# Performance work log

Measured on AMD Instinct MI355X. Metric: run time of the kernel, lower is better.

The kernel has to match this reference:

```python
import jax, jax.numpy as jnp
import numpy as np

N_NODES = 50000
N_EDGES = 800000
IN_C, HID_C, OUT_C = 128, 256, 128


def _gcn_conv(x, src, dst, W, b, num_nodes):
    # PyG GCNConv: self-loops + symmetric normalization + linear + scatter-add
    deg = jax.ops.segment_sum(jnp.ones_like(src, x.dtype), dst, num_segments=num_nodes)
    dinv = jnp.where(deg > 0, jax.lax.rsqrt(deg), 0.0)
    norm = dinv[src] * dinv[dst]                      # [E']
    h = x @ W.T                                       # [N, C_out] transform first (C_out usually < C_in path cost)
    msg = h[src] * norm[:, None]                      # [E', C_out] gather + scale
    out = jax.ops.segment_sum(msg, dst, num_segments=num_nodes)  # scatter-add
    return out + b


def setup_inputs() -> dict:
    key = jax.random.key(0)
    k1, k2, k3, k4 = jax.random.split(key, 4)
    x = jax.random.normal(k1, (N_NODES, IN_C), dtype=jnp.float32)
    edge_index = jax.random.randint(k2, (2, N_EDGES), 0, N_NODES, dtype=jnp.int64)
    W1 = jax.random.normal(k3, (HID_C, IN_C), dtype=jnp.float32) * (1.0 / np.sqrt(IN_C))
    b1 = jnp.zeros((HID_C,), dtype=jnp.float32)
    W2 = jax.random.normal(k4, (OUT_C, HID_C), dtype=jnp.float32) * (1.0 / np.sqrt(HID_C))
    b2 = jnp.zeros((OUT_C,), dtype=jnp.float32)
    return {"x": x, "edge_index": edge_index, "W1": W1, "b1": b1,
            "W2": W2, "b2": b2, "num_nodes": N_NODES}


def reference(x, edge_index, W1, b1, W2, b2, num_nodes):
    # add self-loops once (shared by both layers)
    loop = jnp.arange(num_nodes, dtype=edge_index.dtype)
    src = jnp.concatenate([edge_index[0], loop])
    dst = jnp.concatenate([edge_index[1], loop])
    h = _gcn_conv(x, src, dst, W1, b1, num_nodes)
    h = jax.nn.relu(h)
    out = _gcn_conv(h, src, dst, W2, b2, num_nodes)
    return out
```

## Files before the change

kernel.cpp:

```cpp
#include <hip/hip_runtime.h>

#define N_NODES 50000
#define N_EDGES 800000
#define IN_C 128
#define HID_C 256
#define OUT_C 128
#define NBLK 196
#define NPART 8
#define NREP 8
#define REP_W (N_EDGES / NREP)
#define EB 3125
#define XCONV_BLKS 6250
#define WCONV_BLKS 64

typedef __attribute__((ext_vector_type(8))) short short8v;
typedef __attribute__((ext_vector_type(4))) float f32x4;

static __device__ __forceinline__ unsigned short f2bf(float f) {
  unsigned int u = __float_as_uint(f);
  unsigned int r = (u + 0x7fffu + ((u >> 16) & 1u)) >> 16;
  return (unsigned short)r;
}
static __device__ __forceinline__ float bf2f(unsigned short h) {
  return __uint_as_float(((unsigned int)h) << 16);
}
static __device__ __forceinline__ unsigned int packBF2(float a, float b) {
  return (unsigned int)f2bf(a) | ((unsigned int)f2bf(b) << 16);
}

__global__ __launch_bounds__(256) void deg_zero_k(int* __restrict__ deg8) {
  const int i = blockIdx.x * 256 + threadIdx.x;
  if (i < NREP * N_NODES) deg8[i] = 0;
}

__global__ __launch_bounds__(256) void convert_conv_k(
    const int* __restrict__ ei, uint2* __restrict__ edata, int* __restrict__ deg8,
    const float* __restrict__ x, unsigned int* __restrict__ xbf,
    const float* __restrict__ W1, unsigned int* __restrict__ w1bf,
    const float* __restrict__ W2, unsigned int* __restrict__ w2bf) {
  const int b = blockIdx.x;
  if (b < EB) {
    __shared__ int s_is64;
    if (threadIdx.x == 0) {
      int nz = 0;
#pragma unroll
      for (int k = 0; k < 64; ++k) nz |= ei[2 * k + 1];
      s_is64 = (nz == 0) ? 1 : 0;
    }
    __syncthreads();
    const int is64 = s_is64;
    const int e = b * 256 + threadIdx.x;
    if (e < N_EDGES) {
      int s, d;
      if (is64) {
        const uint2 sv = ((const uint2*)ei)[e];
        const uint2 dv = ((const uint2*)ei)[N_EDGES + e];
        s = (int)sv.x;
        d = (int)dv.x;
      } else {
        s = ei[e];
        d = ei[N_EDGES + e];
      }
      const int rep = e / REP_W;
      const int lrank = atomicAdd(&deg8[rep * N_NODES + d], 1);
      const uint2 t = {(unsigned int)d | ((unsigned int)lrank << 16) |
                           ((unsigned int)rep << 29),
                       (unsigned int)s};
      edata[e] = t;
    }
  } else if (b < EB + XCONV_BLKS) {
    const int i = (b - EB) * 256 + threadIdx.x;
    const float4 f = *(const float4*)(x + (long)i * 4);
    uint2 u = {packBF2(f.x, f.y), packBF2(f.z, f.w)};
    *(uint2*)(xbf + (long)i * 2) = u;
  } else if (b < EB + XCONV_BLKS + WCONV_BLKS) {
    const int i = (b - EB - XCONV_BLKS) * 256 + threadIdx.x;
    const float2 f = *(const float2*)(W1 + (long)i * 2);
    w1bf[i] = packBF2(f.x, f.y);
  } else {
    const int i = (b - EB - XCONV_BLKS - WCONV_BLKS) * 256 + threadIdx.x;
    const float2 f = *(const float2*)(W2 + (long)i * 2);
    w2bf[i] = packBF2(f.x, f.y);
  }
}

__global__ __launch_bounds__(256) void bsum_k(const int* __restrict__ deg8,
                                              int* __restrict__ bsum) {
  const int i = blockIdx.x * 256 + threadIdx.x;
  int v = 0;
  if (i < N_NODES) {
#pragma unroll
    for (int r = 0; r < NREP; ++r) v += deg8[r * N_NODES + i];
  }
#pragma unroll
  for (int off = 32; off > 0; off >>= 1) v += __shfl_down(v, off, 64);
  __shared__ int ws[4];
  if ((threadIdx.x & 63) == 0) ws[threadIdx.x >> 6] = v;
  __syncthreads();
  if (threadIdx.x == 0) bsum[blockIdx.x] = ws[0] + ws[1] + ws[2] + ws[3];
}

__global__ __launch_bounds__(256) void bscan_k(const int* __restrict__ bsum,
                                               int* __restrict__ boff) {
  __shared__ int s[256];
  const int t = threadIdx.x;
  const int v = (t < NBLK) ? bsum[t] : 0;
  s[t] = v;
  __syncthreads();
  for (int off = 1; off < 256; off <<= 1) {
    const int tmp = (t >= off) ? s[t - off] : 0;
    __syncthreads();
    s[t] += tmp;
    __syncthreads();
  }
  if (t < NBLK) boff[t] = s[t] - v;
}

__global__ __launch_bounds__(256) void bfinal_k(const int* __restrict__ deg8,
                                                const int* __restrict__ boff,
                                                int* __restrict__ rowstart,
                                                float* __restrict__ dinv,
                                                int* __restrict__ repoff) {
  __shared__ int s[256];
  const int t = threadIdx.x;
  const int i = blockIdx.x * 256 + t;
  int dr[NREP];
  int dtot = 0;
  if (i < N_NODES) {
#pragma unroll
    for (int r = 0; r < NREP; ++r) {
      dr[r] = deg8[r * N_NODES + i];
      dtot += dr[r];
    }
  }
  s[t] = dtot;
  __syncthreads();
  for (int off = 1; off < 256; off <<= 1) {
    const int tmp = (t >= off) ? s[t - off] : 0;
    __syncthreads();
    s[t] += tmp;
    __syncthreads();
  }
  const int run = boff[blockIdx.x] + s[t] - dtot;
  if (i < N_NODES) {
    rowstart[i] = run;
    dinv[i] = rsqrtf((float)dtot + 1.0f);
    int acc = run;
#pragma unroll
    for (int r = 0; r < NREP; ++r) {
      repoff[i * NREP + r] = acc;
      acc += dr[r];
    }
    if (i == N_NODES - 1) rowstart[N_NODES] = run + dtot;
  }
}

__global__ __launch_bounds__(256) void fill_csr_part_k(const uint2* __restrict__ edata,
                                                       const int* __restrict__ repoff,
                                                       int* __restrict__ csr_src) {
  const int p = blockIdx.x & 7;
  const int e = (blockIdx.x >> 3) * 256 + threadIdx.x;
  if (e < N_EDGES) {
    const uint2 t = edata[e];
    const int d = t.x & 0xffff;
    if (d / 6250 == p) {
      const int lrank = (t.x >> 16) & 0x1fff;
      const int rep = (int)(t.x >> 29);
      csr_src[repoff[d * NREP + rep] + lrank] = (int)t.y;
    }
  }
}

__global__ __launch_bounds__(256) void gemm_fused_k(
    const unsigned int* __restrict__ X,
    const unsigned int* __restrict__ W1BF,
    const float* __restrict__ b1,
    const unsigned int* __restrict__ W2BF,
    unsigned int* __restrict__ outBF) {
  constexpr int KP1 = 68;
  constexpr int HP = 132;
  __shared__ unsigned int xs[64 * KP1];
  __shared__ unsigned int h1s[64 * HP];

  const int tid = threadIdx.x;
  const int w = tid >> 6;
  const int l = tid & 63;
  const long nbase = (long)blockIdx.x * 64;
  const int kg = (l >> 4) * 8;
  const int lr = l & 15;
  const int mq0 = (l >> 4) * 4;

#pragma unroll
  for (int i = 0; i < 4; ++i) {
    const int idx = (tid + i * 256) * 4;
    const int row = idx >> 6, col = idx & 63;
    long gr = nbase + row;
    if (gr > N_NODES - 1) gr = N_NODES - 1;
    const uint4 v = *(const uint4*)(X + gr * 64 + col);
    *(uint4*)(xs + row * KP1 + col) = v;
  }
  __syncthreads();

  {
    const int m0w = w * 64;
    f32x4 acc[4][4];
#pragma unroll
    for (int nt = 0; nt < 4; ++nt)
#pragma unroll
      for (int mt = 0; mt < 4; ++mt) acc[nt][mt] = {0.0f, 0.0f, 0.0f, 0.0f};

#pragma unroll
    for (int ks = 0; ks < 4; ++ks) {
      const int ko = ks * 32 + kg;
      short8v wb[4];
#pragma unroll
      for (int mt = 0; mt < 4; ++mt)
        wb[mt] = *(const short8v*)(W1BF + (long)(m0w + mt * 16 + lr) * (IN_C / 2) +
                                   ko / 2);
#pragma unroll
      for (int nt = 0; nt < 4; ++nt) {
        const short8v xb = *(const short8v*)(xs + (nt * 16 + lr) * KP1 + ko / 2);
#pragma unroll
        for (int mt = 0; mt < 4; ++mt)
          acc[nt][mt] = __builtin_amdgcn_mfma_f32_16x16x32_bf16(wb[mt], xb,
                                                               acc[nt][mt], 0, 0, 0);
      }
    }

#pragma unroll
    for (int nt = 0; nt < 4; ++nt) {
      const int nl = nt * 16 + lr;
#pragma unroll
      for (int mt = 0; mt < 4; ++mt) {
        const int mq = m0w + mt * 16 + mq0;
        const float4 bv = *(const float4*)(b1 + mq);
        const float v0 = fmaxf(acc[nt][mt][0] + bv.x, 0.0f);
        const float v1 = fmaxf(acc[nt][mt][1] + bv.y, 0.0f);
        const float v2 = fmaxf(acc[nt][mt][2] + bv.z, 0.0f);
        const float v3 = fmaxf(acc[nt][mt][3] + bv.w, 0.0f);
        uint2 o = {packBF2(v0, v1), packBF2(v2, v3)};
        *(uint2*)(h1s + nl * HP + mq / 2) = o;
      }
    }
  }
  __syncthreads();

  {
    const int m0w = w * 32;
    f32x4 acc[4][2];
#pragma unroll
    for (int nt = 0; nt < 4; ++nt)
#pragma unroll
      for (int mt = 0; mt < 2; ++mt) acc[nt][mt] = {0.0f, 0.0f, 0.0f, 0.0f};

#pragma unroll
    for (int ks = 0; ks < 8; ++ks) {
      const int ko = ks * 32 + kg;
      short8v wb[2];
#pragma unroll
      for (int mt = 0; mt < 2; ++mt)
        wb[mt] = *(const short8v*)(W2BF + (long)(m0w + mt * 16 + lr) * (HID_C / 2) +
                                   ko / 2);
#pragma unroll
      for (int nt = 0; nt < 4; ++nt) {
        const short8v xb = *(const short8v*)(h1s + (nt * 16 + lr) * HP + ko / 2);
#pragma unroll
        for (int mt = 0; mt < 2; ++mt)
          acc[nt][mt] = __builtin_amdgcn_mfma_f32_16x16x32_bf16(wb[mt], xb,
                                                               acc[nt][mt], 0, 0, 0);
      }
    }

#pragma unroll
    for (int nt = 0; nt < 4; ++nt) {
      const long n = nbase + nt * 16 + lr;
      if (n < N_NODES) {
#pragma unroll
        for (int mt = 0; mt < 2; ++mt) {
          const int mq = m0w + mt * 16 + mq0;
          uint2 o = {packBF2(acc[nt][mt][0], acc[nt][mt][1]),
                     packBF2(acc[nt][mt][2], acc[nt][mt][3])};
          *(uint2*)(outBF + n * (OUT_C / 2) + mq / 2) = o;
        }
      }
    }
  }
}

template <int C, bool HAS_BIAS, bool OUT_BF>
__global__ __launch_bounds__(256) void gather_k(const int* __restrict__ rowstart,
                                                const int* __restrict__ csr_src,
                                                const float* __restrict__ dinv,
                                                const unsigned int* __restrict__ hbf,
                                                const float* __restrict__ bias,
                                                float* __restrict__ out,
                                                unsigned int* __restrict__ outBF) {
  const int v = (blockIdx.x * 256 + threadIdx.x) >> 6;
  if (v >= N_NODES) return;
  const int lane = threadIdx.x & 63;
  constexpr int CW = C / 2;
  const int rs = rowstart[v];
  const int re = rowstart[v + 1];
  const float dv = dinv[v];

  float a0 = 0.0f, a1 = 0.0f;

  int e = rs;
  for (; e + 7 < re; e += 8) {
    int s[8];
    float nn[8];
    unsigned int r[8];
#pragma unroll
    for (int j = 0; j < 8; ++j) s[j] = csr_src[e + j];
#pragma unroll
    for (int j = 0; j < 8; ++j) nn[j] = dv * dinv[s[j]];
#pragma unroll
    for (int j = 0; j < 8; ++j) r[j] = hbf[(long)s[j] * CW + lane];
#pragma unroll
    for (int j = 0; j < 8; ++j) {
      a0 += nn[j] * bf2f((unsigned short)r[j]);
      a1 += nn[j] * bf2f((unsigned short)(r[j] >> 16));
    }
  }
  for (; e + 3 < re; e += 4) {
    int s[4];
    float nn[4];
    unsigned int r[4];
#pragma unroll
    for (int j = 0; j < 4; ++j) s[j] = csr_src[e + j];
#pragma unroll
    for (int j = 0; j < 4; ++j) nn[j] = dv * dinv[s[j]];
#pragma unroll
    for (int j = 0; j < 4; ++j) r[j] = hbf[(long)s[j] * CW + lane];
#pragma unroll
    for (int j = 0; j < 4; ++j) {
      a0 += nn[j] * bf2f((unsigned short)r[j]);
      a1 += nn[j] * bf2f((unsigned short)(r[j] >> 16));
    }
  }
  for (; e < re; ++e) {
    const int s0 = csr_src[e];
    const float n0 = dv * dinv[s0];
    const unsigned int r0 = hbf[(long)s0 * CW + lane];
    a0 += n0 * bf2f((unsigned short)r0);
    a1 += n0 * bf2f((unsigned short)(r0 >> 16));
  }

  const float s2 = dv * dv;
  const unsigned int hv = hbf[(long)v * CW + lane];
  float o0 = s2 * bf2f((unsigned short)hv) + a0;
  float o1 = s2 * bf2f((unsigned short)(hv >> 16)) + a1;
  if (HAS_BIAS) {
    const float2 bv = *(const float2*)(bias + lane * 2);
    o0 += bv.x;
    o1 += bv.y;
  }
  if (OUT_BF) {
    outBF[(long)v * CW + lane] = packBF2(o0, o1);
  } else {
    const float2 o = {o0, o1};
    *(float2*)(out + (long)v * CW * 2 + lane * 2) = o;
  }
}

extern "C" void kernel_launch(void* const* d_in, const int* in_sizes, int n_in,
                              void* d_out, int out_size, void* d_ws, size_t ws_size,
                              hipStream_t stream) {
  (void)in_sizes; (void)n_in; (void)out_size; (void)ws_size;

  const float* x  = (const float*)d_in[0];
  const int*   ei = (const int*)d_in[1];
  const float* W1 = (const float*)d_in[2];
  const float* b1 = (const float*)d_in[3];
  const float* W2 = (const float*)d_in[4];
  const float* b2 = (const float*)d_in[5];
  float* out = (float*)d_out;

  char* ws = (char*)d_ws;
  uint2* edata    = (uint2*)(ws + 0);
  int*   csr_src  = (int*)(ws + 6400000);
  int*   deg8     = (int*)(ws + 9600000);
  int*   rowstart = (int*)(ws + 11200000);
  float* dinv     = (float*)(ws + 11400016);
  int*   bsum     = (int*)(ws + 11600016);
  int*   boff     = (int*)(ws + 11601040);
  int*   repoff   = (int*)(ws + 11700000);
  unsigned int* w1bf   = (unsigned int*)(ws + 13400000);
  unsigned int* w2bf   = (unsigned int*)(ws + 13500000);
  unsigned int* aggxbf = (unsigned int*)(ws + 14000000);
  unsigned int* h2bf   = (unsigned int*)(ws + 27000000);
  unsigned int* xbf    = (unsigned int*)(ws + 91200000);

  const int GB = (N_NODES + 3) / 4;

  deg_zero_k<<<(NREP * N_NODES + 255) / 256, 256, 0, stream>>>(deg8);
  convert_conv_k<<<EB + XCONV_BLKS + 2 * WCONV_BLKS, 256, 0, stream>>>(
      ei, edata, deg8, x, xbf, W1, w1bf, W2, w2bf);
  bsum_k<<<NBLK, 256, 0, stream>>>(deg8, bsum);
  bscan_k<<<1, 256, 0, stream>>>(bsum, boff);
  bfinal_k<<<NBLK, 256, 0, stream>>>(deg8, boff, rowstart, dinv, repoff);
  fill_csr_part_k<<<EB * NPART, 256, 0, stream>>>(edata, repoff, csr_src);

  gather_k<IN_C, false, true><<<GB, 256, 0, stream>>>(
      rowstart, csr_src, dinv, xbf, nullptr, nullptr, aggxbf);

  gemm_fused_k<<<(N_NODES + 63) / 64, 256, 0, stream>>>(aggxbf, w1bf, b1, w2bf,
                                                        h2bf);

  gather_k<OUT_C, true, false><<<GB, 256, 0, stream>>>(
      rowstart, csr_src, dinv, h2bf, b2, out, nullptr);
}
```

Measured before the change: 167.8 us.

## Build CSR via destination-partitioned buckets with LDS histograms instead of global atomics

```diff
diff --git a/kernel.cpp b/kernel.cpp
--- a/kernel.cpp
+++ b/kernel.cpp
@@ -7,8 +7,9 @@
 #define OUT_C 128
 #define NBLK 196
 #define NPART 8
-#define NREP 8
-#define REP_W (N_EDGES / NREP)
+#define PART_W 6250
+#define PCAP 110000
+#define KB 16
 #define EB 3125
 #define XCONV_BLKS 6250
 #define WCONV_BLKS 64
@@ -28,19 +29,24 @@
   return (unsigned int)f2bf(a) | ((unsigned int)f2bf(b) << 16);
 }
 
-__global__ __launch_bounds__(256) void deg_zero_k(int* __restrict__ deg8) {
-  const int i = blockIdx.x * 256 + threadIdx.x;
-  if (i < NREP * N_NODES) deg8[i] = 0;
-}
-
-__global__ __launch_bounds__(256) void convert_conv_k(
-    const int* __restrict__ ei, uint2* __restrict__ edata, int* __restrict__ deg8,
+__global__ void zero8_k(int* __restrict__ pcount) {
+  if (threadIdx.x < NPART) pcount[threadIdx.x] = 0;
+}
+
+__global__ __launch_bounds__(256) void partition_conv_k(
+    const int* __restrict__ ei, unsigned int* __restrict__ partbuf,
+    int* __restrict__ pcount,
     const float* __restrict__ x, unsigned int* __restrict__ xbf,
     const float* __restrict__ W1, unsigned int* __restrict__ w1bf,
     const float* __restrict__ W2, unsigned int* __restrict__ w2bf) {
   const int b = blockIdx.x;
   if (b < EB) {
     __shared__ int s_is64;
+    __shared__ int cnt[NPART], base[NPART], cur[NPART];
+    if (threadIdx.x < NPART) {
+      cnt[threadIdx.x] = 0;
+      cur[threadIdx.x] = 0;
+    }
     if (threadIdx.x == 0) {
       int nz = 0;
 #pragma unroll
@@ -50,8 +56,9 @@
     __syncthreads();
     const int is64 = s_is64;
     const int e = b * 256 + threadIdx.x;
-    if (e < N_EDGES) {
-      int s, d;
+    int s = 0, d = 0, p = 0;
+    const bool valid = (e < N_EDGES);
+    if (valid) {
       if (is64) {
         const uint2 sv = ((const uint2*)ei)[e];
         const uint2 dv = ((const uint2*)ei)[N_EDGES + e];
@@ -61,12 +68,20 @@
         s = ei[e];
         d = ei[N_EDGES + e];
       }
-      const int rep = e / REP_W;
-      const int lrank = atomicAdd(&deg8[rep * N_NODES + d], 1);
-      const uint2 t = {(unsigned int)d | ((unsigned int)lrank << 16) |
-                           ((unsigned int)rep << 29),
-                       (unsigned int)s};
-      edata[e] = t;
+      p = d / PART_W;
+      atomicAdd(&cnt[p], 1);
+    }
+    __syncthreads();
+    if (threadIdx.x < NPART)
+      base[threadIdx.x] = atomicAdd(&pcount[threadIdx.x], cnt[threadIdx.x]);
+    __syncthreads();
+    if (valid) {
+      const int o = atomicAdd(&cur[p], 1);
+      const int idx = base[p] + o;
+      if (idx < PCAP) {
+        partbuf[p * PCAP + idx] =
+            (unsigned int)(d - p * PART_W) | ((unsigned int)s << 13);
+      }
     }
   } else if (b < EB + XCONV_BLKS) {
     const int i = (b - EB) * 256 + threadIdx.x;
@@ -84,13 +99,36 @@
   }
 }
 
-__global__ __launch_bounds__(256) void bsum_k(const int* __restrict__ deg8,
+__global__ __launch_bounds__(1024) void hist_k(const unsigned int* __restrict__ partbuf,
+                                               const int* __restrict__ pcount,
+                                               int* __restrict__ H) {
+  const int p = blockIdx.x & 7;
+  const int blk = blockIdx.x >> 3;
+  __shared__ unsigned int hist[PART_W];
+  for (int i = threadIdx.x; i < PART_W; i += 1024) hist[i] = 0;
+  __syncthreads();
+  const int np = pcount[p] < PCAP ? pcount[p] : PCAP;
+  const int chunk = (np + KB - 1) / KB;
+  const int s0 = blk * chunk;
+  int s1 = s0 + chunk;
+  if (s1 > np) s1 = np;
+  const unsigned int* pb = partbuf + p * PCAP;
+  for (int i = s0 + threadIdx.x; i < s1; i += 1024)
+    atomicAdd(&hist[pb[i] & 0x1fffu], 1u);
+  __syncthreads();
+  int* Hrow = H + (p * KB + blk) * PART_W;
+  for (int i = threadIdx.x; i < PART_W; i += 1024) Hrow[i] = (int)hist[i];
+}
+
+__global__ __launch_bounds__(256) void bsum_k(const int* __restrict__ H,
                                               int* __restrict__ bsum) {
   const int i = blockIdx.x * 256 + threadIdx.x;
   int v = 0;
   if (i < N_NODES) {
-#pragma unroll
-    for (int r = 0; r < NREP; ++r) v += deg8[r * N_NODES + i];
+    const int p = i / PART_W, bin = i % PART_W;
+    const int* Hp = H + p * KB * PART_W + bin;
+#pragma unroll
+    for (int blk = 0; blk < KB; ++blk) v += Hp[blk * PART_W];
   }
 #pragma unroll
   for (int off = 32; off > 0; off >>= 1) v += __shfl_down(v, off, 64);
@@ -116,22 +154,21 @@
   if (t < NBLK) boff[t] = s[t] - v;
 }
 
-__global__ __launch_bounds__(256) void bfinal_k(const int* __restrict__ deg8,
+__global__ __launch_bounds__(256) void bfinal_k(int* __restrict__ H,
                                                 const int* __restrict__ boff,
                                                 int* __restrict__ rowstart,
-                                                float* __restrict__ dinv,
-                                                int* __restrict__ repoff) {
+                                                float* __restrict__ dinv) {
   __shared__ int s[256];
   const int t = threadIdx.x;
   const int i = blockIdx.x * 256 + t;
-  int dr[NREP];
   int dtot = 0;
+  int p = 0, bin = 0;
   if (i < N_NODES) {
-#pragma unroll
-    for (int r = 0; r < NREP; ++r) {
-      dr[r] = deg8[r * N_NODES + i];
-      dtot += dr[r];
-    }
+    p = i / PART_W;
+    bin = i % PART_W;
+    int* Hp = H + p * KB * PART_W + bin;
+#pragma unroll
+    for (int blk = 0; blk < KB; ++blk) dtot += Hp[blk * PART_W];
   }
   s[t] = dtot;
   __syncthreads();
@@ -146,28 +183,38 @@
     rowstart[i] = run;
     dinv[i] = rsqrtf((float)dtot + 1.0f);
     int acc = run;
-#pragma unroll
-    for (int r = 0; r < NREP; ++r) {
-      repoff[i * NREP + r] = acc;
-      acc += dr[r];
+    int* Hp = H + p * KB * PART_W + bin;
+#pragma unroll
+    for (int blk = 0; blk < KB; ++blk) {
+      const int c = Hp[blk * PART_W];
+      Hp[blk * PART_W] = acc;
+      acc += c;
     }
     if (i == N_NODES - 1) rowstart[N_NODES] = run + dtot;
   }
 }
 
-__global__ __launch_bounds__(256) void fill_csr_part_k(const uint2* __restrict__ edata,
-                                                       const int* __restrict__ repoff,
-                                                       int* __restrict__ csr_src) {
+__global__ __launch_bounds__(1024) void scatter_k(const unsigned int* __restrict__ partbuf,
+                                                  const int* __restrict__ pcount,
+                                                  const int* __restrict__ H,
+                                                  int* __restrict__ csr_src) {
   const int p = blockIdx.x & 7;
-  const int e = (blockIdx.x >> 3) * 256 + threadIdx.x;
-  if (e < N_EDGES) {
-    const uint2 t = edata[e];
-    const int d = t.x & 0xffff;
-    if (d / 6250 == p) {
-      const int lrank = (t.x >> 16) & 0x1fff;
-      const int rep = (int)(t.x >> 29);
-      csr_src[repoff[d * NREP + rep] + lrank] = (int)t.y;
-    }
+  const int blk = blockIdx.x >> 3;
+  __shared__ unsigned int hist[PART_W];
+  for (int i = threadIdx.x; i < PART_W; i += 1024) hist[i] = 0;
+  __syncthreads();
+  const int np = pcount[p] < PCAP ? pcount[p] : PCAP;
+  const int chunk = (np + KB - 1) / KB;
+  const int s0 = blk * chunk;
+  int s1 = s0 + chunk;
+  if (s1 > np) s1 = np;
+  const unsigned int* pb = partbuf + p * PCAP;
+  const int* Hrow = H + (p * KB + blk) * PART_W;
+  for (int i = s0 + threadIdx.x; i < s1; i += 1024) {
+    const unsigned int u = pb[i];
+    const int ld = (int)(u & 0x1fffu);
+    const int lr = (int)atomicAdd(&hist[ld], 1u);
+    csr_src[Hrow[ld] + lr] = (int)(u >> 13);
   }
 }
 
@@ -377,29 +424,30 @@
   float* out = (float*)d_out;
 
   char* ws = (char*)d_ws;
-  uint2* edata    = (uint2*)(ws + 0);
-  int*   csr_src  = (int*)(ws + 6400000);
-  int*   deg8     = (int*)(ws + 9600000);
-  int*   rowstart = (int*)(ws + 11200000);
-  float* dinv     = (float*)(ws + 11400016);
-  int*   bsum     = (int*)(ws + 11600016);
-  int*   boff     = (int*)(ws + 11601040);
-  int*   repoff   = (int*)(ws + 11700000);
-  unsigned int* w1bf   = (unsigned int*)(ws + 13400000);
-  unsigned int* w2bf   = (unsigned int*)(ws + 13500000);
-  unsigned int* aggxbf = (unsigned int*)(ws + 14000000);
-  unsigned int* h2bf   = (unsigned int*)(ws + 27000000);
+  unsigned int* partbuf = (unsigned int*)(ws + 0);
+  int*   csr_src  = (int*)(ws + 3600000);
+  int*   H        = (int*)(ws + 6800000);
+  int*   pcount   = (int*)(ws + 10000000);
+  int*   rowstart = (int*)(ws + 10000128);
+  float* dinv     = (float*)(ws + 10200640);
+  int*   bsum     = (int*)(ws + 10400640);
+  int*   boff     = (int*)(ws + 10401664);
+  unsigned int* w1bf   = (unsigned int*)(ws + 10500000);
+  unsigned int* w2bf   = (unsigned int*)(ws + 10600000);
+  unsigned int* aggxbf = (unsigned int*)(ws + 11000000);
+  unsigned int* h2bf   = (unsigned int*)(ws + 24000000);
   unsigned int* xbf    = (unsigned int*)(ws + 91200000);
 
   const int GB = (N_NODES + 3) / 4;
 
-  deg_zero_k<<<(NREP * N_NODES + 255) / 256, 256, 0, stream>>>(deg8);
-  convert_conv_k<<<EB + XCONV_BLKS + 2 * WCONV_BLKS, 256, 0, stream>>>(
-      ei, edata, deg8, x, xbf, W1, w1bf, W2, w2bf);
-  bsum_k<<<NBLK, 256, 0, stream>>>(deg8, bsum);
+  zero8_k<<<1, 64, 0, stream>>>(pcount);
+  partition_conv_k<<<EB + XCONV_BLKS + 2 * WCONV_BLKS, 256, 0, stream>>>(
+      ei, partbuf, pcount, x, xbf, W1, w1bf, W2, w2bf);
+  hist_k<<<NPART * KB, 1024, 0, stream>>>(partbuf, pcount, H);
+  bsum_k<<<NBLK, 256, 0, stream>>>(H, bsum);
   bscan_k<<<1, 256, 0, stream>>>(bsum, boff);
-  bfinal_k<<<NBLK, 256, 0, stream>>>(deg8, boff, rowstart, dinv, repoff);
-  fill_csr_part_k<<<EB * NPART, 256, 0, stream>>>(edata, repoff, csr_src);
+  bfinal_k<<<NBLK, 256, 0, stream>>>(H, boff, rowstart, dinv);
+  scatter_k<<<NPART * KB, 1024, 0, stream>>>(partbuf, pcount, H, csr_src);
 
   gather_k<IN_C, false, true><<<GB, 256, 0, stream>>>(
       rowstart, csr_src, dinv, xbf, nullptr, nullptr, aggxbf);
```

After: 167.9 us. No clear change (+0.1%).

## Build CSR with LDS-histogram partitioned counting instead of global atomics

Applied to the files above, without the earlier changes.

```diff
diff --git a/kernel.cpp b/kernel.cpp
--- a/kernel.cpp
+++ b/kernel.cpp
@@ -7,8 +7,9 @@
 #define OUT_C 128
 #define NBLK 196
 #define NPART 8
-#define NREP 8
-#define REP_W (N_EDGES / NREP)
+#define PART_W 6250
+#define KB2 32
+#define CHUNK (N_EDGES / KB2)
 #define EB 3125
 #define XCONV_BLKS 6250
 #define WCONV_BLKS 64
@@ -28,13 +29,8 @@
   return (unsigned int)f2bf(a) | ((unsigned int)f2bf(b) << 16);
 }
 
-__global__ __launch_bounds__(256) void deg_zero_k(int* __restrict__ deg8) {
-  const int i = blockIdx.x * 256 + threadIdx.x;
-  if (i < NREP * N_NODES) deg8[i] = 0;
-}
-
 __global__ __launch_bounds__(256) void convert_conv_k(
-    const int* __restrict__ ei, uint2* __restrict__ edata, int* __restrict__ deg8,
+    const int* __restrict__ ei, unsigned int* __restrict__ edata,
     const float* __restrict__ x, unsigned int* __restrict__ xbf,
     const float* __restrict__ W1, unsigned int* __restrict__ w1bf,
     const float* __restrict__ W2, unsigned int* __restrict__ w2bf) {
@@ -61,12 +57,7 @@
         s = ei[e];
         d = ei[N_EDGES + e];
       }
-      const int rep = e / REP_W;
-      const int lrank = atomicAdd(&deg8[rep * N_NODES + d], 1);
-      const uint2 t = {(unsigned int)d | ((unsigned int)lrank << 16) |
-                           ((unsigned int)rep << 29),
-                       (unsigned int)s};
-      edata[e] = t;
+      edata[e] = (unsigned int)d | ((unsigned int)s << 16);
     }
   } else if (b < EB + XCONV_BLKS) {
     const int i = (b - EB) * 256 + threadIdx.x;
@@ -84,13 +75,33 @@
   }
 }
 
-__global__ __launch_bounds__(256) void bsum_k(const int* __restrict__ deg8,
+__global__ __launch_bounds__(1024) void hist_k(const unsigned int* __restrict__ edata,
+                                               int* __restrict__ H) {
+  const int p = blockIdx.x & 7;
+  const int c = blockIdx.x >> 3;
+  __shared__ unsigned int hist[PART_W];
+  for (int i = threadIdx.x; i < PART_W; i += 1024) hist[i] = 0;
+  __syncthreads();
+  const int s0 = c * CHUNK;
+  for (int i = s0 + threadIdx.x; i < s0 + CHUNK; i += 1024) {
+    const unsigned int u = edata[i];
+    const int d = (int)(u & 0xffffu);
+    if (d / PART_W == p) atomicAdd(&hist[d - p * PART_W], 1u);
+  }
+  __syncthreads();
+  int* Hrow = H + (p * KB2 + c) * PART_W;
+  for (int i = threadIdx.x; i < PART_W; i += 1024) Hrow[i] = (int)hist[i];
+}
+
+__global__ __launch_bounds__(256) void bsum_k(const int* __restrict__ H,
                                               int* __restrict__ bsum) {
   const int i = blockIdx.x * 256 + threadIdx.x;
   int v = 0;
   if (i < N_NODES) {
-#pragma unroll
-    for (int r = 0; r < NREP; ++r) v += deg8[r * N_NODES + i];
+    const int p = i / PART_W, bin = i % PART_W;
+    const int* Hp = H + p * KB2 * PART_W + bin;
+#pragma unroll
+    for (int c = 0; c < KB2; ++c) v += Hp[c * PART_W];
   }
 #pragma unroll
   for (int off = 32; off > 0; off >>= 1) v += __shfl_down(v, off, 64);
@@ -116,22 +127,21 @@
   if (t < NBLK) boff[t] = s[t] - v;
 }
 
-__global__ __launch_bounds__(256) void bfinal_k(const int* __restrict__ deg8,
+__global__ __launch_bounds__(256) void bfinal_k(int* __restrict__ H,
                                                 const int* __restrict__ boff,
                                                 int* __restrict__ rowstart,
-                                                float* __restrict__ dinv,
-                                                int* __restrict__ repoff) {
+                                                float* __restrict__ dinv) {
   __shared__ int s[256];
   const int t = threadIdx.x;
   const int i = blockIdx.x * 256 + t;
-  int dr[NREP];
   int dtot = 0;
+  int p = 0, bin = 0;
   if (i < N_NODES) {
-#pragma unroll
-    for (int r = 0; r < NREP; ++r) {
-      dr[r] = deg8[r * N_NODES + i];
-      dtot += dr[r];
-    }
+    p = i / PART_W;
+    bin = i % PART_W;
+    int* Hp = H + p * KB2 * PART_W + bin;
+#pragma unroll
+    for (int c = 0; c < KB2; ++c) dtot += Hp[c * PART_W];
   }
   s[t] = dtot;
   __syncthreads();
@@ -146,27 +156,34 @@
     rowstart[i] = run;
     dinv[i] = rsqrtf((float)dtot + 1.0f);
     int acc = run;
-#pragma unroll
-    for (int r = 0; r < NREP; ++r) {
-      repoff[i * NREP + r] = acc;
-      acc += dr[r];
+    int* Hp = H + p * KB2 * PART_W + bin;
+#pragma unroll
+    for (int c = 0; c < KB2; ++c) {
+      const int cnt = Hp[c * PART_W];
+      Hp[c * PART_W] = acc;
+      acc += cnt;
     }
     if (i == N_NODES - 1) rowstart[N_NODES] = run + dtot;
   }
 }
 
-__global__ __launch_bounds__(256) void fill_csr_part_k(const uint2* __restrict__ edata,
-                                                       const int* __restrict__ repoff,
-                                                       int* __restrict__ csr_src) {
+__global__ __launch_bounds__(1024) void scatter_k(const unsigned int* __restrict__ edata,
+                                                  const int* __restrict__ H,
+                                                  int* __restrict__ csr_src) {
   const int p = blockIdx.x & 7;
-  const int e = (blockIdx.x >> 3) * 256 + threadIdx.x;
-  if (e < N_EDGES) {
-    const uint2 t = edata[e];
-    const int d = t.x & 0xffff;
-    if (d / 6250 == p) {
-      const int lrank = (t.x >> 16) & 0x1fff;
-      const int rep = (int)(t.x >> 29);
-      csr_src[repoff[d * NREP + rep] + lrank] = (int)t.y;
+  const int c = blockIdx.x >> 3;
+  __shared__ unsigned int hist[PART_W];
+  for (int i = threadIdx.x; i < PART_W; i += 1024) hist[i] = 0;
+  __syncthreads();
+  const int s0 = c * CHUNK;
+  const int* Hrow = H + (p * KB2 + c) * PART_W;
+  for (int i = s0 + threadIdx.x; i < s0 + CHUNK; i += 1024) {
+    const unsigned int u = edata[i];
+    const int d = (int)(u & 0xffffu);
+    if (d / PART_W == p) {
+      const int ld = d - p * PART_W;
+      const int lr = (int)atomicAdd(&hist[ld], 1u);
+      csr_src[Hrow[ld] + lr] = (int)(u >> 16);
     }
   }
 }
@@ -377,29 +394,28 @@
   float* out = (float*)d_out;
 
   char* ws = (char*)d_ws;
-  uint2* edata    = (uint2*)(ws + 0);
-  int*   csr_src  = (int*)(ws + 6400000);
-  int*   deg8     = (int*)(ws + 9600000);
-  int*   rowstart = (int*)(ws + 11200000);
-  float* dinv     = (float*)(ws + 11400016);
-  int*   bsum     = (int*)(ws + 11600016);
-  int*   boff     = (int*)(ws + 11601040);
-  int*   repoff   = (int*)(ws + 11700000);
-  unsigned int* w1bf   = (unsigned int*)(ws + 13400000);
-  unsigned int* w2bf   = (unsigned int*)(ws + 13500000);
+  unsigned int* edata = (unsigned int*)(ws + 0);
+  int*   csr_src  = (int*)(ws + 3200000);
+  int*   H        = (int*)(ws + 6400000);
+  int*   rowstart = (int*)(ws + 12800000);
+  float* dinv     = (float*)(ws + 13000512);
+  int*   bsum     = (int*)(ws + 13200512);
+  int*   boff     = (int*)(ws + 13201536);
+  unsigned int* w1bf   = (unsigned int*)(ws + 13300000);
+  unsigned int* w2bf   = (unsigned int*)(ws + 13400000);
   unsigned int* aggxbf = (unsigned int*)(ws + 14000000);
   unsigned int* h2bf   = (unsigned int*)(ws + 27000000);
   unsigned int* xbf    = (unsigned int*)(ws + 91200000);
 
   const int GB = (N_NODES + 3) / 4;
 
-  deg_zero_k<<<(NREP * N_NODES + 255) / 256, 256, 0, stream>>>(deg8);
   convert_conv_k<<<EB + XCONV_BLKS + 2 * WCONV_BLKS, 256, 0, stream>>>(
-      ei, edata, deg8, x, xbf, W1, w1bf, W2, w2bf);
-  bsum_k<<<NBLK, 256, 0, stream>>>(deg8, bsum);
+      ei, edata, x, xbf, W1, w1bf, W2, w2bf);
+  hist_k<<<NPART * KB2, 1024, 0, stream>>>(edata, H);
+  bsum_k<<<NBLK, 256, 0, stream>>>(H, bsum);
   bscan_k<<<1, 256, 0, stream>>>(bsum, boff);
-  bfinal_k<<<NBLK, 256, 0, stream>>>(deg8, boff, rowstart, dinv, repoff);
-  fill_csr_part_k<<<EB * NPART, 256, 0, stream>>>(edata, repoff, csr_src);
+  bfinal_k<<<NBLK, 256, 0, stream>>>(H, boff, rowstart, dinv);
+  scatter_k<<<NPART * KB2, 1024, 0, stream>>>(edata, H, csr_src);
 
   gather_k<IN_C, false, true><<<GB, 256, 0, stream>>>(
       rowstart, csr_src, dinv, xbf, nullptr, nullptr, aggxbf);
```

Result: faster. 153.1 us (-8.7%).
